# Kernel tuning notes

Measured on AMD Instinct MI355X. Metric: run time of the kernel, lower is better.

## Reference

```python
import jax, jax.numpy as jnp
import numpy as np


def square_distance(src, dst):
    # src: [B,N,C], dst: [B,M,C] -> [B,N,M] squared euclidean distances
    # ||s||^2 + ||d||^2 - 2 s.d, same expansion as the torch module
    d = -2.0 * jnp.einsum('bnc,bmc->bnm', src, dst)
    d = d + jnp.sum(src * src, axis=-1)[:, :, None]
    d = d + jnp.sum(dst * dst, axis=-1)[:, None, :]
    return d


def setup_inputs() -> dict:
    key = jax.random.key(0)
    k1, k2 = jax.random.split(key)
    B, N, M, C = 32, 4096, 4096, 3
    x = jax.random.normal(k1, (B, N, C), dtype=jnp.float32)
    recon = jax.random.normal(k2, (B, M, C), dtype=jnp.float32)
    return {"x": x, "recon": recon}


def reference(x, recon):
    # Chamfer distance (get_loss). square_distance(recon, x) is the
    # transpose of square_distance(x, recon), so compute once.
    d = square_distance(x, recon)            # [B,N,M]
    cost_p2_p1 = jnp.min(d, axis=-1)         # min over recon for each x point
    cost_p1_p2 = jnp.min(d, axis=-2)         # min over x for each recon point
    loss = jnp.mean(cost_p1_p2) + jnp.mean(cost_p2_p1)
    return loss
```

## Files before the change

### kernel.cpp

```cpp
#include <hip/hip_runtime.h>
#include <float.h>
#include <stdint.h>


typedef short bf16x8 __attribute__((ext_vector_type(8)));
typedef float f32x16 __attribute__((ext_vector_type(16)));

#define BLK 256
#define ONE_BF 0x3F80u

__device__ __forceinline__ uint32_t bf16_rne(float f) {
    uint32_t u = __builtin_bit_cast(uint32_t, f);
    return (u + 0x7FFFu + ((u >> 16) & 1u)) >> 16;
}
__device__ __forceinline__ float bf16f(uint32_t h) {
    return __builtin_bit_cast(float, h << 16);
}

__global__ __launch_bounds__(BLK)
void prep_kernel(const float* __restrict__ x, const float* __restrict__ recon,
                 uint32_t* __restrict__ ws, float* __restrict__ out)
{
    int tid = blockIdx.x * BLK + threadIdx.x;
    if (tid == 0) out[0] = 0.0f;
    int arr = tid >> 17;
    int p   = tid & 131071;
    const float* s = arr ? recon : x;
    float a = s[3 * p], b = s[3 * p + 1], c = s[3 * p + 2];
    uint32_t hx = bf16_rne(a), hy = bf16_rne(b), hz = bf16_rne(c);
    uint32_t lx = bf16_rne(a - bf16f(hx));
    uint32_t ly = bf16_rne(b - bf16f(hy));
    uint32_t lz = bf16_rne(c - bf16f(hz));
    float tt = a * a + b * b + c * c;
    uint32_t th = bf16_rne(tt);
    uint32_t tl = bf16_rne(tt - bf16f(th));
    uint4 H0 = make_uint4(hx | (hy << 16), hz | (hx << 16),
                          hy | (hz << 16), lx | (ly << 16));
    uint4 H1 = make_uint4(lz | (th << 16), tl | (lx << 16),
                          ly | (lz << 16), 0u);
    ((uint4*)ws)[tid]          = H0;
    ((uint4*)ws)[262144 + tid] = H1;
}

__global__ __launch_bounds__(BLK, 3)
void chamfer_mfma(const float* __restrict__ x, const float* __restrict__ recon,
                  const uint32_t* __restrict__ ws, float* __restrict__ out,
                  float scale)
{
    int idx = blockIdx.x;
    int swz = (idx & 7) * 128 + (idx >> 3);
    int dir = swz >> 9;
    int b   = (swz >> 4) & 31;
    int qb  = swz & 15;

    const float* qsrc = dir ? recon : x;
    const int arrT = dir ? 0 : 1;

    const int tid  = threadIdx.x;
    const int wave = tid >> 6;
    const int lane = tid & 63;
    const int l31  = lane & 31;
    const int lh   = lane >> 5;

    bf16x8 A0, A1;
    {
        int n0 = qb * 256 + wave * 64 + l31;
        #pragma unroll
        for (int rb = 0; rb < 2; ++rb) {
            const float* qp = qsrc + ((size_t)b * 4096 + n0 + rb * 32) * 3;
            float cx = -2.f * qp[0], cy = -2.f * qp[1], cz = -2.f * qp[2];
            uint32_t hx = bf16_rne(cx), hy = bf16_rne(cy), hz = bf16_rne(cz);
            uint32_t lx = bf16_rne(cx - bf16f(hx));
            uint32_t ly = bf16_rne(cy - bf16f(hy));
            uint32_t lz = bf16_rne(cz - bf16f(hz));
            uint32_t w0, w1, w2, w3;
            if (lh == 0) {
                w0 = hx | (hy << 16); w1 = hz | (lx << 16);
                w2 = ly | (lz << 16); w3 = hx | (hy << 16);
            } else {
                w0 = hz | (ONE_BF << 16); w1 = ONE_BF | (lx << 16);
                w2 = ly | (lz << 16);     w3 = 0u;
            }
            union { uint4 u; bf16x8 v; } cvt;
            cvt.u = make_uint4(w0, w1, w2, w3);
            if (rb == 0) A0 = cvt.v; else A1 = cvt.v;
        }
    }

    f32x16 zc = {0,0,0,0,0,0,0,0,0,0,0,0,0,0,0,0};
    float rmn0[16], rmn1[16];
    #pragma unroll
    for (int j = 0; j < 16; ++j) { rmn0[j] = FLT_MAX; rmn1[j] = FLT_MAX; }

    const uint4* rp = (const uint4*)ws
        + (size_t)lh * 262144 + (size_t)arrT * 131072 + (size_t)b * 4096 + l31;

    for (int it = 0; it < 64; ++it) {
        union BU { uint4 u; bf16x8 v; } B0, B1;
        B0.u = rp[0];
        B1.u = rp[32];
        rp += 64;
        f32x16 d0 = __builtin_amdgcn_mfma_f32_32x32x16_bf16(A0, B0.v, zc, 0, 0, 0);
        f32x16 d1 = __builtin_amdgcn_mfma_f32_32x32x16_bf16(A0, B1.v, zc, 0, 0, 0);
        #pragma unroll
        for (int j = 0; j < 16; ++j)
            rmn0[j] = fminf(rmn0[j], fminf(d0[j], d1[j]));
        f32x16 e0 = __builtin_amdgcn_mfma_f32_32x32x16_bf16(A1, B0.v, zc, 0, 0, 0);
        f32x16 e1 = __builtin_amdgcn_mfma_f32_32x32x16_bf16(A1, B1.v, zc, 0, 0, 0);
        #pragma unroll
        for (int j = 0; j < 16; ++j)
            rmn1[j] = fminf(rmn1[j], fminf(e0[j], e1[j]));
    }

    __shared__ float lmin[256][33];
    #pragma unroll
    for (int j = 0; j < 16; ++j) {
        int rl = (j & 3) + 8 * (j >> 2) + 4 * lh;
        lmin[wave * 64 + rl][l31]      = rmn0[j];
        lmin[wave * 64 + 32 + rl][l31] = rmn1[j];
    }
    __syncthreads();

    float m = lmin[tid][0];
    #pragma unroll
    for (int c = 1; c < 32; ++c) m = fminf(m, lmin[tid][c]);

    const float* qp = qsrc + ((size_t)b * 4096 + qb * 256 + tid) * 3;
    float v = m + qp[0] * qp[0] + qp[1] * qp[1] + qp[2] * qp[2];

    #pragma unroll
    for (int off = 32; off > 0; off >>= 1)
        v += __shfl_down(v, off, 64);
    __shared__ float red[4];
    if (lane == 0) red[wave] = v;
    __syncthreads();
    if (tid == 0)
        atomicAdd(out, (red[0] + red[1] + red[2] + red[3]) * scale);
}

extern "C" void kernel_launch(void* const* d_in, const int* in_sizes, int n_in,
                              void* d_out, int out_size, void* d_ws, size_t ws_size,
                              hipStream_t stream) {
    const float* x     = (const float*)d_in[0];
    const float* recon = (const float*)d_in[1];
    float* out = (float*)d_out;

    const float scale = 1.0f / (32.0f * 4096.0f);

    prep_kernel<<<1024, BLK, 0, stream>>>(x, recon, (uint32_t*)d_ws, out);

    chamfer_mfma<<<1024, BLK, 0, stream>>>(x, recon, (const uint32_t*)d_ws,
                                           out, scale);
}
```

Baseline: 100.9 us.

## Split target range across two blocks and reduce partial minima in a separate kernel

The main MFMA kernel is templated so each block scans only half of the target points (TH=2). This doubles the grid to 2048 blocks to improve occupancy and tail balance. Per-query partial minima are now reduced across lanes with shuffles instead of an LDS transpose, then written to workspace. A new reduce kernel takes the min of the two halves, sums, and does the atomic add. This adds a kernel launch and extra workspace traffic, and it depends on the workspace being large enough, with the original kernel kept as a fallback.

```diff
diff --git a/kernel.cpp b/kernel.cpp
--- a/kernel.cpp
+++ b/kernel.cpp
@@ -42,16 +42,17 @@
     ((uint4*)ws)[262144 + tid] = H1;
 }
 
-__global__ __launch_bounds__(BLK, 3)
-void chamfer_mfma(const float* __restrict__ x, const float* __restrict__ recon,
-                  const uint32_t* __restrict__ ws, float* __restrict__ out,
-                  float scale)
+template <int TH>
+__global__ __launch_bounds__(BLK)
+void chamfer_mfma_p(const float* __restrict__ x, const float* __restrict__ recon,
+                    const uint32_t* __restrict__ ws, float* __restrict__ ws2)
 {
     int idx = blockIdx.x;
-    int swz = (idx & 7) * 128 + (idx >> 3);
-    int dir = swz >> 9;
-    int b   = (swz >> 4) & 31;
-    int qb  = swz & 15;
+    constexpr int CPX = 1024 * TH / 8;
+    int swz = (idx & 7) * CPX + (idx >> 3);
+    int th, qb, b, dir;
+    if (TH == 2) { th = swz & 1;  qb = (swz >> 1) & 15; b = (swz >> 5) & 31; dir = swz >> 10; }
+    else         { th = 0;        qb = swz & 15;        b = (swz >> 4) & 31; dir = swz >> 9;  }
 
     const float* qsrc = dir ? recon : x;
     const int arrT = dir ? 0 : 1;
@@ -93,9 +94,11 @@
     for (int j = 0; j < 16; ++j) { rmn0[j] = FLT_MAX; rmn1[j] = FLT_MAX; }
 
     const uint4* rp = (const uint4*)ws
-        + (size_t)lh * 262144 + (size_t)arrT * 131072 + (size_t)b * 4096 + l31;
-
-    for (int it = 0; it < 64; ++it) {
+        + (size_t)lh * 262144 + (size_t)arrT * 131072 + (size_t)b * 4096
+        + (size_t)th * (2048 / TH) * TH + l31;
+
+    constexpr int ITERS = 64 / TH;
+    for (int it = 0; it < ITERS; ++it) {
         union BU { uint4 u; bf16x8 v; } B0, B1;
         B0.u = rp[0];
         B1.u = rp[32];
@@ -112,6 +115,113 @@
             rmn1[j] = fminf(rmn1[j], fminf(e0[j], e1[j]));
     }
 
+    #pragma unroll
+    for (int j = 0; j < 16; ++j) {
+        float a = rmn0[j], c = rmn1[j];
+        #pragma unroll
+        for (int mk = 16; mk >= 1; mk >>= 1) {
+            a = fminf(a, __shfl_xor(a, mk, 64));
+            c = fminf(c, __shfl_xor(c, mk, 64));
+        }
+        rmn0[j] = a; rmn1[j] = c;
+    }
+
+    int n0 = qb * 256 + wave * 64 + l31;
+    const float* qp0 = qsrc + ((size_t)b * 4096 + n0) * 3;
+    float q2_0 = qp0[0]*qp0[0] + qp0[1]*qp0[1] + qp0[2]*qp0[2];
+    float q2_1 = qp0[96]*qp0[96] + qp0[97]*qp0[97] + qp0[98]*qp0[98];
+    size_t base = (((size_t)th * 2 + dir) * 32 + b) * 4096
+                + (size_t)qb * 256 + (size_t)wave * 64;
+    #pragma unroll
+    for (int j = 0; j < 16; ++j) {
+        int r = (j & 3) + 8 * (j >> 2) + 4 * lh;
+        if (l31 == r) {
+            ws2[base + r]      = rmn0[j] + q2_0;
+            ws2[base + 32 + r] = rmn1[j] + q2_1;
+        }
+    }
+}
+
+__global__ __launch_bounds__(BLK)
+void chamfer_reduce(const float* __restrict__ ws2, float* __restrict__ out,
+                    int two_halves, float scale)
+{
+    int q = blockIdx.x * BLK + threadIdx.x;
+    float v = ws2[q];
+    if (two_halves) v = fminf(v, ws2[262144 + q]);
+
+    #pragma unroll
+    for (int off = 32; off > 0; off >>= 1)
+        v += __shfl_down(v, off, 64);
+
+    __shared__ float red[4];
+    int tid = threadIdx.x;
+    if ((tid & 63) == 0) red[tid >> 6] = v;
+    __syncthreads();
+    if (tid == 0) {
+        float s = red[0] + red[1] + red[2] + red[3];
+        atomicAdd(out, s * scale);
+    }
+}
+
+__global__ __launch_bounds__(BLK, 3)
+void chamfer_mfma_full(const float* __restrict__ x, const float* __restrict__ recon,
+                       const uint32_t* __restrict__ ws, float* __restrict__ out,
+                       float scale)
+{
+    int idx = blockIdx.x;
+    int swz = (idx & 7) * 128 + (idx >> 3);
+    int dir = swz >> 9;
+    int b   = (swz >> 4) & 31;
+    int qb  = swz & 15;
+    const float* qsrc = dir ? recon : x;
+    const int arrT = dir ? 0 : 1;
+    const int tid  = threadIdx.x;
+    const int wave = tid >> 6;
+    const int lane = tid & 63;
+    const int l31  = lane & 31;
+    const int lh   = lane >> 5;
+    bf16x8 A0, A1;
+    {
+        int n0 = qb * 256 + wave * 64 + l31;
+        #pragma unroll
+        for (int rb = 0; rb < 2; ++rb) {
+            const float* qp = qsrc + ((size_t)b * 4096 + n0 + rb * 32) * 3;
+            float cx = -2.f * qp[0], cy = -2.f * qp[1], cz = -2.f * qp[2];
+            uint32_t hx = bf16_rne(cx), hy = bf16_rne(cy), hz = bf16_rne(cz);
+            uint32_t lx = bf16_rne(cx - bf16f(hx));
+            uint32_t ly = bf16_rne(cy - bf16f(hy));
+            uint32_t lz = bf16_rne(cz - bf16f(hz));
+            uint32_t w0, w1, w2, w3;
+            if (lh == 0) { w0 = hx | (hy << 16); w1 = hz | (lx << 16);
+                           w2 = ly | (lz << 16); w3 = hx | (hy << 16); }
+            else         { w0 = hz | (ONE_BF << 16); w1 = ONE_BF | (lx << 16);
+                           w2 = ly | (lz << 16);     w3 = 0u; }
+            union { uint4 u; bf16x8 v; } cvt;
+            cvt.u = make_uint4(w0, w1, w2, w3);
+            if (rb == 0) A0 = cvt.v; else A1 = cvt.v;
+        }
+    }
+    f32x16 zc = {0,0,0,0,0,0,0,0,0,0,0,0,0,0,0,0};
+    float rmn0[16], rmn1[16];
+    #pragma unroll
+    for (int j = 0; j < 16; ++j) { rmn0[j] = FLT_MAX; rmn1[j] = FLT_MAX; }
+    const uint4* rp = (const uint4*)ws
+        + (size_t)lh * 262144 + (size_t)arrT * 131072 + (size_t)b * 4096 + l31;
+    for (int it = 0; it < 64; ++it) {
+        union BU { uint4 u; bf16x8 v; } B0, B1;
+        B0.u = rp[0]; B1.u = rp[32]; rp += 64;
+        f32x16 d0 = __builtin_amdgcn_mfma_f32_32x32x16_bf16(A0, B0.v, zc, 0, 0, 0);
+        f32x16 d1 = __builtin_amdgcn_mfma_f32_32x32x16_bf16(A0, B1.v, zc, 0, 0, 0);
+        #pragma unroll
+        for (int j = 0; j < 16; ++j)
+            rmn0[j] = fminf(rmn0[j], fminf(d0[j], d1[j]));
+        f32x16 e0 = __builtin_amdgcn_mfma_f32_32x32x16_bf16(A1, B0.v, zc, 0, 0, 0);
+        f32x16 e1 = __builtin_amdgcn_mfma_f32_32x32x16_bf16(A1, B1.v, zc, 0, 0, 0);
+        #pragma unroll
+        for (int j = 0; j < 16; ++j)
+            rmn1[j] = fminf(rmn1[j], fminf(e0[j], e1[j]));
+    }
     __shared__ float lmin[256][33];
     #pragma unroll
     for (int j = 0; j < 16; ++j) {
@@ -120,14 +230,11 @@
         lmin[wave * 64 + 32 + rl][l31] = rmn1[j];
     }
     __syncthreads();
-
     float m = lmin[tid][0];
     #pragma unroll
     for (int c = 1; c < 32; ++c) m = fminf(m, lmin[tid][c]);
-
     const float* qp = qsrc + ((size_t)b * 4096 + qb * 256 + tid) * 3;
     float v = m + qp[0] * qp[0] + qp[1] * qp[1] + qp[2] * qp[2];
-
     #pragma unroll
     for (int off = 32; off > 0; off >>= 1)
         v += __shfl_down(v, off, 64);
@@ -144,11 +251,20 @@
     const float* x     = (const float*)d_in[0];
     const float* recon = (const float*)d_in[1];
     float* out = (float*)d_out;
+    uint32_t* ws = (uint32_t*)d_ws;
+    float* ws2 = (float*)((char*)d_ws + (size_t)8 * 1024 * 1024);
 
     const float scale = 1.0f / (32.0f * 4096.0f);
 
-    prep_kernel<<<1024, BLK, 0, stream>>>(x, recon, (uint32_t*)d_ws, out);
-
-    chamfer_mfma<<<1024, BLK, 0, stream>>>(x, recon, (const uint32_t*)d_ws,
-                                           out, scale);
-}
+    prep_kernel<<<1024, BLK, 0, stream>>>(x, recon, ws, out);
+
+    if (ws_size >= (size_t)10 * 1024 * 1024 + 512 * 1024) {
+        chamfer_mfma_p<2><<<2048, BLK, 0, stream>>>(x, recon, ws, ws2);
+        chamfer_reduce<<<1024, BLK, 0, stream>>>(ws2, out, 1, scale);
+    } else if (ws_size >= (size_t)9 * 1024 * 1024 + 256 * 1024) {
+        chamfer_mfma_p<1><<<1024, BLK, 0, stream>>>(x, recon, ws, ws2);
+        chamfer_reduce<<<1024, BLK, 0, stream>>>(ws2, out, 0, scale);
+    } else {
+        chamfer_mfma_full<<<1024, BLK, 0, stream>>>(x, recon, ws, out, scale);
+    }
+}
```

After: 133.8 us. +32.6%, slower.

## Compute both Chamfer directions in one pass with shared and global atomicMin column minima

Applied to the files above, without the earlier changes.

The distance matrix is now computed once per batch instead of twice, once per direction. Row minima are reduced in registers, and column minima are gathered per iteration through shared-memory atomicMin on float bits clamped to be non-negative, then merged into a global buffer. The query squared norm is folded into the MFMA operand so the full distance comes out of the matrix unit, and a third kernel sums the row and column minima. The aim is to halve the MFMA work. In exchange it adds per-iteration folds, shuffles, shared atomics, an extra kernel launch, and only 512 blocks.

```diff
diff --git a/kernel.cpp b/kernel.cpp
--- a/kernel.cpp
+++ b/kernel.cpp
@@ -16,17 +16,25 @@
 __device__ __forceinline__ float bf16f(uint32_t h) {
     return __builtin_bit_cast(float, h << 16);
 }
+__device__ __forceinline__ float fold16(f32x16 v) {
+    float a0 = fminf(v[0], v[1]),   a1 = fminf(v[2], v[3]);
+    float a2 = fminf(v[4], v[5]),   a3 = fminf(v[6], v[7]);
+    float a4 = fminf(v[8], v[9]),   a5 = fminf(v[10], v[11]);
+    float a6 = fminf(v[12], v[13]), a7 = fminf(v[14], v[15]);
+    a0 = fminf(a0, a1); a2 = fminf(a2, a3);
+    a4 = fminf(a4, a5); a6 = fminf(a6, a7);
+    return fminf(fminf(a0, a2), fminf(a4, a6));
+}
 
 __global__ __launch_bounds__(BLK)
-void prep_kernel(const float* __restrict__ x, const float* __restrict__ recon,
-                 uint32_t* __restrict__ ws, float* __restrict__ out)
+void prep_kernel(const float* __restrict__ recon,
+                 uint32_t* __restrict__ wrec, uint32_t* __restrict__ gcol,
+                 float* __restrict__ out)
 {
     int tid = blockIdx.x * BLK + threadIdx.x;
     if (tid == 0) out[0] = 0.0f;
-    int arr = tid >> 17;
-    int p   = tid & 131071;
-    const float* s = arr ? recon : x;
-    float a = s[3 * p], b = s[3 * p + 1], c = s[3 * p + 2];
+    gcol[tid] = 0x7F800000u;
+    float a = recon[3 * tid], b = recon[3 * tid + 1], c = recon[3 * tid + 2];
     uint32_t hx = bf16_rne(a), hy = bf16_rne(b), hz = bf16_rne(c);
     uint32_t lx = bf16_rne(a - bf16f(hx));
     uint32_t ly = bf16_rne(b - bf16f(hy));
@@ -37,24 +45,20 @@
     uint4 H0 = make_uint4(hx | (hy << 16), hz | (hx << 16),
                           hy | (hz << 16), lx | (ly << 16));
     uint4 H1 = make_uint4(lz | (th << 16), tl | (lx << 16),
-                          ly | (lz << 16), 0u);
-    ((uint4*)ws)[tid]          = H0;
-    ((uint4*)ws)[262144 + tid] = H1;
-}
-
-__global__ __launch_bounds__(BLK, 3)
-void chamfer_mfma(const float* __restrict__ x, const float* __restrict__ recon,
-                  const uint32_t* __restrict__ ws, float* __restrict__ out,
-                  float scale)
+                          ly | (lz << 16), ONE_BF | (ONE_BF << 16));
+    ((uint4*)wrec)[tid]          = H0;
+    ((uint4*)wrec)[131072 + tid] = H1;
+}
+
+__global__ __launch_bounds__(BLK)
+void chamfer_mfma(const float* __restrict__ x,
+                  const uint32_t* __restrict__ wrec,
+                  float* __restrict__ wrow, uint32_t* __restrict__ gcol)
 {
     int idx = blockIdx.x;
-    int swz = (idx & 7) * 128 + (idx >> 3);
-    int dir = swz >> 9;
-    int b   = (swz >> 4) & 31;
+    int swz = (idx & 7) * 64 + (idx >> 3);
     int qb  = swz & 15;
-
-    const float* qsrc = dir ? recon : x;
-    const int arrT = dir ? 0 : 1;
+    int b   = swz >> 4;
 
     const int tid  = threadIdx.x;
     const int wave = tid >> 6;
@@ -62,38 +66,48 @@
     const int l31  = lane & 31;
     const int lh   = lane >> 5;
 
+    __shared__ unsigned colmin[4096];
+    __shared__ float lmin[256][17];
+
+    for (int k = tid; k < 4096; k += BLK) colmin[k] = 0x7F800000u;
+
     bf16x8 A0, A1;
     {
         int n0 = qb * 256 + wave * 64 + l31;
         #pragma unroll
         for (int rb = 0; rb < 2; ++rb) {
-            const float* qp = qsrc + ((size_t)b * 4096 + n0 + rb * 32) * 3;
-            float cx = -2.f * qp[0], cy = -2.f * qp[1], cz = -2.f * qp[2];
+            const float* qp = x + ((size_t)b * 4096 + n0 + rb * 32) * 3;
+            float ax = qp[0], ay = qp[1], az = qp[2];
+            float q2 = ax * ax + ay * ay + az * az;
+            float cx = -2.f * ax, cy = -2.f * ay, cz = -2.f * az;
             uint32_t hx = bf16_rne(cx), hy = bf16_rne(cy), hz = bf16_rne(cz);
             uint32_t lx = bf16_rne(cx - bf16f(hx));
             uint32_t ly = bf16_rne(cy - bf16f(hy));
             uint32_t lz = bf16_rne(cz - bf16f(hz));
+            uint32_t qh = bf16_rne(q2);
+            uint32_t ql = bf16_rne(q2 - bf16f(qh));
             uint32_t w0, w1, w2, w3;
             if (lh == 0) {
                 w0 = hx | (hy << 16); w1 = hz | (lx << 16);
                 w2 = ly | (lz << 16); w3 = hx | (hy << 16);
             } else {
                 w0 = hz | (ONE_BF << 16); w1 = ONE_BF | (lx << 16);
-                w2 = ly | (lz << 16);     w3 = 0u;
+                w2 = ly | (lz << 16);     w3 = qh | (ql << 16);
             }
             union { uint4 u; bf16x8 v; } cvt;
             cvt.u = make_uint4(w0, w1, w2, w3);
             if (rb == 0) A0 = cvt.v; else A1 = cvt.v;
         }
     }
+    __syncthreads();
 
     f32x16 zc = {0,0,0,0,0,0,0,0,0,0,0,0,0,0,0,0};
     float rmn0[16], rmn1[16];
     #pragma unroll
     for (int j = 0; j < 16; ++j) { rmn0[j] = FLT_MAX; rmn1[j] = FLT_MAX; }
 
-    const uint4* rp = (const uint4*)ws
-        + (size_t)lh * 262144 + (size_t)arrT * 131072 + (size_t)b * 4096 + l31;
+    const uint4* rp = (const uint4*)wrec
+        + (size_t)lh * 131072 + (size_t)b * 4096 + l31;
 
     for (int it = 0; it < 64; ++it) {
         union BU { uint4 u; bf16x8 v; } B0, B1;
@@ -105,37 +119,67 @@
         #pragma unroll
         for (int j = 0; j < 16; ++j)
             rmn0[j] = fminf(rmn0[j], fminf(d0[j], d1[j]));
+        float f0 = fold16(d0);
+        float f1 = fold16(d1);
         f32x16 e0 = __builtin_amdgcn_mfma_f32_32x32x16_bf16(A1, B0.v, zc, 0, 0, 0);
         f32x16 e1 = __builtin_amdgcn_mfma_f32_32x32x16_bf16(A1, B1.v, zc, 0, 0, 0);
         #pragma unroll
         for (int j = 0; j < 16; ++j)
             rmn1[j] = fminf(rmn1[j], fminf(e0[j], e1[j]));
-    }
-
-    __shared__ float lmin[256][33];
+        f0 = fminf(f0, fold16(e0));
+        f1 = fminf(f1, fold16(e1));
+        f0 = fminf(f0, __shfl_xor(f0, 32, 64));
+        f1 = fminf(f1, __shfl_xor(f1, 32, 64));
+        f0 = fmaxf(f0, 0.0f);
+        f1 = fmaxf(f1, 0.0f);
+        if (lh == 0) {
+            int m = it * 64 + l31;
+            atomicMin(&colmin[m],      __float_as_uint(f0));
+            atomicMin(&colmin[m + 32], __float_as_uint(f1));
+        }
+    }
+
     #pragma unroll
     for (int j = 0; j < 16; ++j) {
         int rl = (j & 3) + 8 * (j >> 2) + 4 * lh;
-        lmin[wave * 64 + rl][l31]      = rmn0[j];
-        lmin[wave * 64 + 32 + rl][l31] = rmn1[j];
+        float a = fminf(rmn0[j], __shfl_xor(rmn0[j], 16, 64));
+        float c = fminf(rmn1[j], __shfl_xor(rmn1[j], 16, 64));
+        lmin[wave * 64 + rl][l31 & 15]      = a;
+        lmin[wave * 64 + 32 + rl][l31 & 15] = c;
     }
     __syncthreads();
 
     float m = lmin[tid][0];
     #pragma unroll
-    for (int c = 1; c < 32; ++c) m = fminf(m, lmin[tid][c]);
-
-    const float* qp = qsrc + ((size_t)b * 4096 + qb * 256 + tid) * 3;
-    float v = m + qp[0] * qp[0] + qp[1] * qp[1] + qp[2] * qp[2];
+    for (int c = 1; c < 16; ++c) m = fminf(m, lmin[tid][c]);
+    wrow[(size_t)b * 4096 + qb * 256 + tid] = fmaxf(m, 0.0f);
+
+    uint32_t* g = gcol + (size_t)b * 4096;
+    #pragma unroll
+    for (int k = 0; k < 16; ++k)
+        atomicMin(&g[k * 256 + tid], colmin[k * 256 + tid]);
+}
+
+__global__ __launch_bounds__(BLK)
+void chamfer_reduce(const float* __restrict__ wrow,
+                    const uint32_t* __restrict__ gcol,
+                    float* __restrict__ out, float scale)
+{
+    int q = blockIdx.x * BLK + threadIdx.x;
+    float v = wrow[q] + __uint_as_float(gcol[q]);
 
     #pragma unroll
     for (int off = 32; off > 0; off >>= 1)
         v += __shfl_down(v, off, 64);
+
     __shared__ float red[4];
-    if (lane == 0) red[wave] = v;
+    int tid = threadIdx.x;
+    if ((tid & 63) == 0) red[tid >> 6] = v;
     __syncthreads();
-    if (tid == 0)
-        atomicAdd(out, (red[0] + red[1] + red[2] + red[3]) * scale);
+    if (tid == 0) {
+        float s = red[0] + red[1] + red[2] + red[3];
+        atomicAdd(out, s * scale);
+    }
 }
 
 extern "C" void kernel_launch(void* const* d_in, const int* in_sizes, int n_in,
@@ -145,10 +189,13 @@
     const float* recon = (const float*)d_in[1];
     float* out = (float*)d_out;
 
+    uint32_t* wrec = (uint32_t*)d_ws;
+    float*    wrow = (float*)((char*)d_ws + (size_t)4 * 1024 * 1024);
+    uint32_t* gcol = (uint32_t*)((char*)d_ws + (size_t)4608 * 1024);
+
     const float scale = 1.0f / (32.0f * 4096.0f);
 
-    prep_kernel<<<1024, BLK, 0, stream>>>(x, recon, (uint32_t*)d_ws, out);
-
-    chamfer_mfma<<<1024, BLK, 0, stream>>>(x, recon, (const uint32_t*)d_ws,
-                                           out, scale);
-}
+    prep_kernel<<<512, BLK, 0, stream>>>(recon, wrec, gcol, out);
+    chamfer_mfma<<<512, BLK, 0, stream>>>(x, wrec, wrow, gcol);
+    chamfer_reduce<<<512, BLK, 0, stream>>>(wrow, gcol, out, scale);
+}
```

New measurement: 124.2 us. 1.23x slower.

## Halve per-block query tile to 128 rows and double grid size

Applied to the files above, without the earlier changes.

Each wave now handles one 32-row query tile instead of two, so a block covers 128 query points and the grid grows to 2048 blocks. The per-lane min registers are halved and the cross-lane reduction uses a shuffle before a smaller shared-memory pass. The min-occupancy launch bound is dropped. This trades lower register use and better load balance against half the reuse of each loaded reference fragment, so reference traffic through the workspace doubles.

```diff
diff --git a/kernel.cpp b/kernel.cpp
--- a/kernel.cpp
+++ b/kernel.cpp
@@ -42,16 +42,16 @@
     ((uint4*)ws)[262144 + tid] = H1;
 }
 
-__global__ __launch_bounds__(BLK, 3)
+__global__ __launch_bounds__(BLK)
 void chamfer_mfma(const float* __restrict__ x, const float* __restrict__ recon,
                   const uint32_t* __restrict__ ws, float* __restrict__ out,
                   float scale)
 {
     int idx = blockIdx.x;
-    int swz = (idx & 7) * 128 + (idx >> 3);
-    int dir = swz >> 9;
-    int b   = (swz >> 4) & 31;
-    int qb  = swz & 15;
+    int swz = (idx & 7) * 256 + (idx >> 3);
+    int qb  = swz & 31;
+    int b   = (swz >> 5) & 31;
+    int dir = swz >> 10;
 
     const float* qsrc = dir ? recon : x;
     const int arrT = dir ? 0 : 1;
@@ -62,35 +62,35 @@
     const int l31  = lane & 31;
     const int lh   = lane >> 5;
 
-    bf16x8 A0, A1;
+    __shared__ float lmin[128][17];
+    __shared__ float red[2];
+
+    bf16x8 A0;
     {
-        int n0 = qb * 256 + wave * 64 + l31;
-        #pragma unroll
-        for (int rb = 0; rb < 2; ++rb) {
-            const float* qp = qsrc + ((size_t)b * 4096 + n0 + rb * 32) * 3;
-            float cx = -2.f * qp[0], cy = -2.f * qp[1], cz = -2.f * qp[2];
-            uint32_t hx = bf16_rne(cx), hy = bf16_rne(cy), hz = bf16_rne(cz);
-            uint32_t lx = bf16_rne(cx - bf16f(hx));
-            uint32_t ly = bf16_rne(cy - bf16f(hy));
-            uint32_t lz = bf16_rne(cz - bf16f(hz));
-            uint32_t w0, w1, w2, w3;
-            if (lh == 0) {
-                w0 = hx | (hy << 16); w1 = hz | (lx << 16);
-                w2 = ly | (lz << 16); w3 = hx | (hy << 16);
-            } else {
-                w0 = hz | (ONE_BF << 16); w1 = ONE_BF | (lx << 16);
-                w2 = ly | (lz << 16);     w3 = 0u;
-            }
-            union { uint4 u; bf16x8 v; } cvt;
-            cvt.u = make_uint4(w0, w1, w2, w3);
-            if (rb == 0) A0 = cvt.v; else A1 = cvt.v;
+        int n0 = qb * 128 + wave * 32 + l31;
+        const float* qp = qsrc + ((size_t)b * 4096 + n0) * 3;
+        float cx = -2.f * qp[0], cy = -2.f * qp[1], cz = -2.f * qp[2];
+        uint32_t hx = bf16_rne(cx), hy = bf16_rne(cy), hz = bf16_rne(cz);
+        uint32_t lx = bf16_rne(cx - bf16f(hx));
+        uint32_t ly = bf16_rne(cy - bf16f(hy));
+        uint32_t lz = bf16_rne(cz - bf16f(hz));
+        uint32_t w0, w1, w2, w3;
+        if (lh == 0) {
+            w0 = hx | (hy << 16); w1 = hz | (lx << 16);
+            w2 = ly | (lz << 16); w3 = hx | (hy << 16);
+        } else {
+            w0 = hz | (ONE_BF << 16); w1 = ONE_BF | (lx << 16);
+            w2 = ly | (lz << 16);     w3 = 0u;
         }
+        union { uint4 u; bf16x8 v; } cvt;
+        cvt.u = make_uint4(w0, w1, w2, w3);
+        A0 = cvt.v;
     }
 
     f32x16 zc = {0,0,0,0,0,0,0,0,0,0,0,0,0,0,0,0};
-    float rmn0[16], rmn1[16];
+    float rmn[16];
     #pragma unroll
-    for (int j = 0; j < 16; ++j) { rmn0[j] = FLT_MAX; rmn1[j] = FLT_MAX; }
+    for (int j = 0; j < 16; ++j) rmn[j] = FLT_MAX;
 
     const uint4* rp = (const uint4*)ws
         + (size_t)lh * 262144 + (size_t)arrT * 131072 + (size_t)b * 4096 + l31;
@@ -104,38 +104,33 @@
         f32x16 d1 = __builtin_amdgcn_mfma_f32_32x32x16_bf16(A0, B1.v, zc, 0, 0, 0);
         #pragma unroll
         for (int j = 0; j < 16; ++j)
-            rmn0[j] = fminf(rmn0[j], fminf(d0[j], d1[j]));
-        f32x16 e0 = __builtin_amdgcn_mfma_f32_32x32x16_bf16(A1, B0.v, zc, 0, 0, 0);
-        f32x16 e1 = __builtin_amdgcn_mfma_f32_32x32x16_bf16(A1, B1.v, zc, 0, 0, 0);
-        #pragma unroll
-        for (int j = 0; j < 16; ++j)
-            rmn1[j] = fminf(rmn1[j], fminf(e0[j], e1[j]));
+            rmn[j] = fminf(rmn[j], fminf(d0[j], d1[j]));
     }
 
-    __shared__ float lmin[256][33];
     #pragma unroll
     for (int j = 0; j < 16; ++j) {
         int rl = (j & 3) + 8 * (j >> 2) + 4 * lh;
-        lmin[wave * 64 + rl][l31]      = rmn0[j];
-        lmin[wave * 64 + 32 + rl][l31] = rmn1[j];
+        float a = fminf(rmn[j], __shfl_xor(rmn[j], 16, 64));
+        lmin[wave * 32 + rl][l31 & 15] = a;
     }
     __syncthreads();
 
-    float m = lmin[tid][0];
-    #pragma unroll
-    for (int c = 1; c < 32; ++c) m = fminf(m, lmin[tid][c]);
-
-    const float* qp = qsrc + ((size_t)b * 4096 + qb * 256 + tid) * 3;
-    float v = m + qp[0] * qp[0] + qp[1] * qp[1] + qp[2] * qp[2];
+    float v = 0.0f;
+    if (tid < 128) {
+        float m = lmin[tid][0];
+        #pragma unroll
+        for (int c = 1; c < 16; ++c) m = fminf(m, lmin[tid][c]);
+        const float* qp = qsrc + ((size_t)b * 4096 + qb * 128 + tid) * 3;
+        v = m + qp[0] * qp[0] + qp[1] * qp[1] + qp[2] * qp[2];
+    }
 
     #pragma unroll
     for (int off = 32; off > 0; off >>= 1)
         v += __shfl_down(v, off, 64);
-    __shared__ float red[4];
-    if (lane == 0) red[wave] = v;
+    if (lane == 0 && wave < 2) red[wave] = v;
     __syncthreads();
     if (tid == 0)
-        atomicAdd(out, (red[0] + red[1] + red[2] + red[3]) * scale);
+        atomicAdd(out, (red[0] + red[1]) * scale);
 }
 
 extern "C" void kernel_launch(void* const* d_in, const int* in_sizes, int n_in,
@@ -144,11 +139,10 @@
     const float* x     = (const float*)d_in[0];
     const float* recon = (const float*)d_in[1];
     float* out = (float*)d_out;
+    uint32_t* ws = (uint32_t*)d_ws;
 
     const float scale = 1.0f / (32.0f * 4096.0f);
 
-    prep_kernel<<<1024, BLK, 0, stream>>>(x, recon, (uint32_t*)d_ws, out);
-
-    chamfer_mfma<<<1024, BLK, 0, stream>>>(x, recon, (const uint32_t*)d_ws,
-                                           out, scale);
+    prep_kernel<<<1024, BLK, 0, stream>>>(x, recon, ws, out);
+    chamfer_mfma<<<2048, BLK, 0, stream>>>(x, recon, ws, out, scale);
 }
```

Result: slower. 143.3 us (+42.0%).
